# Kernel optimization log

Measured on AMD Instinct MI355X. Metric: run time of the kernel, lower is better.

## Reference

```python
import jax, jax.numpy as jnp
import numpy as np
from jax import lax

PCR = (-59.9, -59.9, -2.0, 59.9, 59.9, 5.9)
TOPK = 10
THRESHOLD = 0.5
MARGIN = 0.5
EPS = 1e-8  # torch cosine_similarity default eps


def setup_inputs() -> dict:
    key = jax.random.key(0)
    k1, k2, k3, k4, k5 = jax.random.split(key, 5)
    B, C, H, W, N = 4, 64, 512, 512, 30
    loc_features = jax.random.normal(k1, (B, C, H, W), dtype=jnp.float32)
    det_features = jax.random.normal(k2, (B, C, H, W), dtype=jnp.float32)
    # gt boxes: x,y inside point-cloud range; last element is class id (0 == static)
    xy = jax.random.uniform(k3, (B, N, 2), minval=-55.0, maxval=55.0, dtype=jnp.float32)
    rest = jax.random.normal(k4, (B, N, 5), dtype=jnp.float32)
    cls = jax.random.randint(k5, (B, N, 1), 0, 3).astype(jnp.float32)
    gt_boxes = jnp.concatenate([xy, rest, cls], axis=-1)  # [B, N, 8]
    return {"loc_features": loc_features, "det_features": det_features, "gt_boxes": gt_boxes}


def _loss_fwd(loc_features, det_features, gt_boxes):
    B, C, H, W = loc_features.shape
    bw = PCR[3] - PCR[0]
    bh = PCR[4] - PCR[1]

    def per_batch(loc_fm, det_fm, boxes):
        # --- static GT detection features (gather at box centers) ---
        static_mask = boxes[:, -1] == 0  # [N]
        cx = jnp.clip(((boxes[:, 0] - PCR[0]) / bw * W).astype(jnp.int32), 0, W - 1)
        cy = jnp.clip(((boxes[:, 1] - PCR[1]) / bh * H).astype(jnp.int32), 0, H - 1)
        det_feats = det_fm[:, cy, cx].T  # [N, C]

        # --- find_peaks: local-max of L2 intensity, threshold, top-k (stop-grad) ---
        intensity = lax.stop_gradient(jnp.sqrt(jnp.sum(loc_fm * loc_fm, axis=0)))  # [H, W]
        pooled = lax.reduce_window(intensity, -jnp.inf, lax.max, (3, 3), (1, 1), [(1, 1), (1, 1)])
        peak_mask = (intensity == pooled) & (intensity > THRESHOLD)
        masked = jnp.where(peak_mask, intensity, -jnp.inf).reshape(-1)
        vals, idx = lax.top_k(masked, TOPK)  # descending by intensity
        valid_peak = jnp.isfinite(vals)  # handles < TOPK peaks
        py, px = idx // W, idx % W
        peak_feats = loc_fm[:, py, px].T  # [K, C]

        # --- pairwise cosine similarity (torch eps semantics) ---
        dn = det_feats / jnp.maximum(jnp.linalg.norm(det_feats, axis=-1, keepdims=True), EPS)
        pn = peak_feats / jnp.maximum(jnp.linalg.norm(peak_feats, axis=-1, keepdims=True), EPS)
        sim = jnp.einsum('nc,kc->nk', dn, pn)  # [N, K]

        pair_mask = (static_mask[:, None] & valid_peak[None, :]).astype(sim.dtype)
        n_pairs = jnp.sum(pair_mask)
        loss_sum = jnp.sum(jax.nn.relu(sim - MARGIN) * pair_mask)
        return jnp.where(n_pairs > 0, loss_sum / jnp.maximum(n_pairs, 1.0), 0.0)

    losses = jax.vmap(per_batch)(loc_features, det_features, gt_boxes)  # [B]
    return jnp.sum(losses) / B


def reference(loc_features, det_features, gt_boxes):
    return _loss_fwd(loc_features, det_features, gt_boxes)
```

## Files before the change

kernel.cpp:

```cpp
#include <hip/hip_runtime.h>
#include <math.h>

typedef unsigned long long u64;
typedef unsigned int u32;
typedef float f4 __attribute__((ext_vector_type(4)));

#define HH 512
#define WW 512
#define CC 64
#define HWHW (HH * WW)
#define NBOX 30
#define KTOP 10
#define BLKS_PER_B 256
#define CAND_PER_BATCH (BLKS_PER_B * KTOP)

__device__ __forceinline__ u64 umax64(u64 a, u64 b) { return a > b ? a : b; }
__device__ __forceinline__ u64 umin64(u64 a, u64 b) { return a > b ? b : a; }

__device__ __forceinline__ void merge10(u64 lv[KTOP], const u64* B) {
    u64 c[16];
    #pragma unroll
    for (int i = 0; i < 16; ++i) {
        u64 a = (i < KTOP) ? lv[i] : 0ull;
        u64 b = (i >= 6) ? B[15 - i] : 0ull;
        c[i] = umax64(a, b);
    }
    #pragma unroll
    for (int s = 8; s >= 1; s >>= 1) {
        #pragma unroll
        for (int i = 0; i < 16; ++i) {
            if ((i & s) == 0) {
                u64 lo = c[i], hi = c[i | s];
                c[i] = umax64(lo, hi);
                c[i | s] = umin64(lo, hi);
            }
        }
    }
    #pragma unroll
    for (int i = 0; i < KTOP; ++i) lv[i] = c[i];
}

__global__ void k_intensity(const float* __restrict__ loc, float* __restrict__ inten) {
    int t   = threadIdx.x;
    int blk = blockIdx.x;
    int b   = blk >> 7;
    int j   = blk & 127;
    const f4* base = reinterpret_cast<const f4*>(loc + (size_t)b * CC * HWHW);
    int q0 = j * 512 + t;
    int q1 = q0 + 256;

    f4 s0 = {0.f, 0.f, 0.f, 0.f};
    f4 s1 = {0.f, 0.f, 0.f, 0.f};
    #pragma unroll 8
    for (int c = 0; c < CC; ++c) {
        const f4* p = base + (size_t)c * (HWHW / 4);
        f4 v0 = __builtin_nontemporal_load(p + q0);
        f4 v1 = __builtin_nontemporal_load(p + q1);
        s0 += v0 * v0;
        s1 += v1 * v1;
    }
    f4 o0, o1;
    o0[0] = sqrtf(s0[0]); o0[1] = sqrtf(s0[1]); o0[2] = sqrtf(s0[2]); o0[3] = sqrtf(s0[3]);
    o1[0] = sqrtf(s1[0]); o1[1] = sqrtf(s1[1]); o1[2] = sqrtf(s1[2]); o1[3] = sqrtf(s1[3]);
    f4* out = reinterpret_cast<f4*>(inten + (size_t)b * HWHW);
    out[q0] = o0;
    out[q1] = o1;
}

__global__ void k_peakblock(const float* __restrict__ inten, u64* __restrict__ cand) {
    int t    = threadIdx.x;
    int lane = t & 63;
    int blk  = blockIdx.x;
    int b    = blk >> 8;
    int pblk = blk & 255;
    const float* I = inten + (size_t)b * HWHW;
    int pix0 = pblk * 1024 + t * 4;
    int y  = pix0 >> 9;
    int x0 = pix0 & (WW - 1);

    float w00,w01,w02,w03,w04,w05, w10,w11,w12,w13,w14,w15, w20,w21,w22,w23,w24,w25;
    {
        bool r0 = (y - 1) >= 0, r2 = (y + 1) < HH;
        bool c0 = (x0 - 1) >= 0, c5 = (x0 + 4) < WW;
        const float* Rm = I + (y - 1) * WW + x0;
        const float* Rc = I + y * WW + x0;
        const float* Rp = I + (y + 1) * WW + x0;
        w00 = (r0 && c0) ? Rm[-1] : -INFINITY;
        w01 = r0 ? Rm[0] : -INFINITY;  w02 = r0 ? Rm[1] : -INFINITY;
        w03 = r0 ? Rm[2] : -INFINITY;  w04 = r0 ? Rm[3] : -INFINITY;
        w05 = (r0 && c5) ? Rm[4] : -INFINITY;
        w10 = c0 ? Rc[-1] : -INFINITY;
        w11 = Rc[0]; w12 = Rc[1]; w13 = Rc[2]; w14 = Rc[3];
        w15 = c5 ? Rc[4] : -INFINITY;
        w20 = (r2 && c0) ? Rp[-1] : -INFINITY;
        w21 = r2 ? Rp[0] : -INFINITY;  w22 = r2 ? Rp[1] : -INFINITY;
        w23 = r2 ? Rp[2] : -INFINITY;  w24 = r2 ? Rp[3] : -INFINITY;
        w25 = (r2 && c5) ? Rp[4] : -INFINITY;
    }

    u64 k0, k1, k2, k3;
    {
        float m, v;
        v = w11;
        m = fmaxf(fmaxf(fmaxf(w00, w01), fmaxf(w02, w10)),
                  fmaxf(fmaxf(w11, w12), fmaxf(fmaxf(w20, w21), w22)));
        k0 = (v > 0.5f && v == m) ? (((u64)(__float_as_uint(v) | 0x80000000u) << 32) | (u32)(~(u32)(pix0 + 0))) : 0ull;
        v = w12;
        m = fmaxf(fmaxf(fmaxf(w01, w02), fmaxf(w03, w11)),
                  fmaxf(fmaxf(w12, w13), fmaxf(fmaxf(w21, w22), w23)));
        k1 = (v > 0.5f && v == m) ? (((u64)(__float_as_uint(v) | 0x80000000u) << 32) | (u32)(~(u32)(pix0 + 1))) : 0ull;
        v = w13;
        m = fmaxf(fmaxf(fmaxf(w02, w03), fmaxf(w04, w12)),
                  fmaxf(fmaxf(w13, w14), fmaxf(fmaxf(w22, w23), w24)));
        k2 = (v > 0.5f && v == m) ? (((u64)(__float_as_uint(v) | 0x80000000u) << 32) | (u32)(~(u32)(pix0 + 2))) : 0ull;
        v = w14;
        m = fmaxf(fmaxf(fmaxf(w03, w04), fmaxf(w05, w13)),
                  fmaxf(fmaxf(w14, w15), fmaxf(fmaxf(w23, w24), w25)));
        k3 = (v > 0.5f && v == m) ? (((u64)(__float_as_uint(v) | 0x80000000u) << 32) | (u32)(~(u32)(pix0 + 3))) : 0ull;
    }

    u64 a[4]; int n = 0;
    if (k0) a[n++] = k0;
    if (k1) a[n++] = k1;
    if (k2) a[n++] = k2;
    if (k3) a[n++] = k3;

    __shared__ int cnt;
    __shared__ u64 pool[1024];
    __shared__ u64 smb[64][KTOP];
    if (t == 0) cnt = 0;
    __syncthreads();

    int incl = n;
    #pragma unroll
    for (int s = 1; s < 64; s <<= 1) {
        int o = __shfl_up(incl, s, 64);
        if (lane >= s) incl += o;
    }
    int excl = incl - n;
    int wtot = __shfl(incl, 63, 64);
    int base = 0;
    if (lane == 0 && wtot > 0) base = atomicAdd(&cnt, wtot);
    base = __shfl(base, 0, 64);
    for (int i = 0; i < n; ++i) pool[base + excl + i] = a[i];
    __syncthreads();

    int total = cnt;
    if (t < 64) {
        u64 lv[KTOP];
        #pragma unroll
        for (int i = 0; i < KTOP; ++i) lv[i] = 0ull;
        for (int j = lane; j < total; j += 64) {
            u64 v = pool[j];
            if (v > lv[KTOP - 1]) {
                lv[KTOP - 1] = v;
                #pragma unroll
                for (int m = KTOP - 1; m > 0; --m)
                    if (lv[m] > lv[m - 1]) { u64 tm = lv[m]; lv[m] = lv[m - 1]; lv[m - 1] = tm; }
            }
        }
        #pragma unroll
        for (int i = 0; i < KTOP; ++i) smb[lane][i] = lv[i];
        #pragma unroll
        for (int half = 32; half >= 1; half >>= 1) {
            if (lane < half) {
                merge10(lv, &smb[lane + half][0]);
                #pragma unroll
                for (int i = 0; i < KTOP; ++i) smb[lane][i] = lv[i];
            }
        }
        if (lane == 0) {
            u64* out = cand + (size_t)b * CAND_PER_BATCH + (size_t)pblk * KTOP;
            #pragma unroll
            for (int i = 0; i < KTOP; ++i) out[i] = lv[i];
        }
    }
}

__global__ void k_loss(const float* __restrict__ loc, const float* __restrict__ det,
                       const float* __restrict__ boxes,
                       const u64* __restrict__ cand,
                       float* __restrict__ bloss) {
    int b = blockIdx.x;
    int t = threadIdx.x;

    u64 lv[KTOP];
    #pragma unroll
    for (int i = 0; i < KTOP; ++i) lv[i] = 0ull;
    const u64* C = cand + (size_t)b * CAND_PER_BATCH;
    #pragma unroll
    for (int w = 0; w < CAND_PER_BATCH / 256; ++w) {
        u64 v = C[t + w * 256];
        if (v > lv[KTOP - 1]) {
            lv[KTOP - 1] = v;
            #pragma unroll
            for (int m = KTOP - 1; m > 0; --m)
                if (lv[m] > lv[m - 1]) { u64 tm = lv[m]; lv[m] = lv[m - 1]; lv[m - 1] = tm; }
        }
    }

    __shared__ u64 mb[256][KTOP];
    #pragma unroll
    for (int i = 0; i < KTOP; ++i) mb[t][i] = lv[i];
    __syncthreads();
    for (int half = 128; half >= 1; half >>= 1) {
        if (t < half) {
            merge10(lv, &mb[t + half][0]);
            #pragma unroll
            for (int i = 0; i < KTOP; ++i) mb[t][i] = lv[i];
        }
        __syncthreads();
    }

    __shared__ int topi[KTOP], tvalid[KTOP];
    if (t < KTOP) {
        u64 kk = mb[0][t];
        tvalid[t] = (kk != 0ull) ? 1 : 0;
        topi[t] = (int)((~(u32)kk) & (HWHW - 1));
    }

    __shared__ int s_cx[NBOX], s_cy[NBOX], s_static[NBOX];
    if (t < NBOX) {
        const float* bx = boxes + ((size_t)b * NBOX + t) * 8;
        float fx = (bx[0] + 59.9f) / 119.8f * 512.0f;
        float fy = (bx[1] + 59.9f) / 119.8f * 512.0f;
        int cx = (int)fx; int cy = (int)fy;
        cx = min(max(cx, 0), WW - 1);
        cy = min(max(cy, 0), HH - 1);
        s_cx[t] = cx; s_cy[t] = cy;
        s_static[t] = (bx[7] == 0.0f) ? 1 : 0;
    }
    __syncthreads();

    __shared__ float pf[KTOP][CC];
    __shared__ float df[NBOX][CC];
    #pragma unroll
    for (int w = 0; w < 3; ++w) {
        int e = t + w * 256;
        if (e < KTOP * CC) {
            int k = e >> 6, c = e & 63;
            int pix = tvalid[k] ? topi[k] : 0;
            pf[k][c] = loc[((size_t)b * CC + c) * HWHW + pix];
        }
    }
    #pragma unroll
    for (int w = 0; w < 8; ++w) {
        int e = t + w * 256;
        if (e < NBOX * CC) {
            int n = e >> 6, c = e & 63;
            int pix = s_cy[n] * WW + s_cx[n];
            df[n][c] = det[((size_t)b * CC + c) * HWHW + pix];
        }
    }
    __syncthreads();

    __shared__ float invn[NBOX + KTOP];
    if (t < NBOX + KTOP) {
        float s = 0.f;
        if (t < NBOX) {
            for (int c = 0; c < CC; ++c) s += df[t][c] * df[t][c];
        } else {
            int k = t - NBOX;
            for (int c = 0; c < CC; ++c) s += pf[k][c] * pf[k][c];
        }
        invn[t] = 1.0f / fmaxf(sqrtf(s), 1e-8f);
    }
    __syncthreads();
    for (int e = t; e < NBOX * CC; e += 256) { int n = e >> 6; df[n][e & 63] *= invn[n]; }
    for (int e = t; e < KTOP * CC; e += 256) { int k = e >> 6; pf[k][e & 63] *= invn[NBOX + k]; }
    __syncthreads();

    float lsum = 0.f, cntp = 0.f;
    for (int p = t; p < NBOX * KTOP; p += 256) {
        int n = p / KTOP, k = p - n * KTOP;
        float dot = 0.f;
        for (int c = 0; c < CC; ++c) dot += df[n][c] * pf[k][c];
        if (s_static[n] && tvalid[k]) {
            float r = dot - 0.5f;
            if (r > 0.f) lsum += r;
            cntp += 1.f;
        }
    }
    __shared__ float hv[256];
    __shared__ float hc[256];
    hv[t] = lsum; hc[t] = cntp;
    __syncthreads();
    for (int s = 128; s > 0; s >>= 1) {
        if (t < s) { hv[t] += hv[t + s]; hc[t] += hc[t + s]; }
        __syncthreads();
    }
    if (t == 0) {
        float np = hc[0];
        bloss[b] = (np > 0.f) ? hv[0] / fmaxf(np, 1.0f) : 0.f;
    }
}

__global__ void k_final(const float* __restrict__ bloss, float* __restrict__ out, int B) {
    float s = 0.f;
    for (int b = 0; b < B; ++b) s += bloss[b];
    out[0] = s / (float)B;
}

extern "C" void kernel_launch(void* const* d_in, const int* in_sizes, int n_in,
                              void* d_out, int out_size, void* d_ws, size_t ws_size,
                              hipStream_t stream) {
    const float* loc   = (const float*)d_in[0];
    const float* det   = (const float*)d_in[1];
    const float* boxes = (const float*)d_in[2];
    float* out = (float*)d_out;

    int B = in_sizes[0] / (CC * HWHW);

    float* inten = (float*)d_ws;
    u64*   cand  = (u64*)(inten + (size_t)B * HWHW);
    float* bloss = (float*)(cand + (size_t)B * CAND_PER_BATCH);

    dim3 blk(256);
    int g1 = B * 128;
    hipLaunchKernelGGL(k_intensity, dim3(g1), blk, 0, stream, loc, inten);
    hipLaunchKernelGGL(k_peakblock, dim3(B * BLKS_PER_B), blk, 0, stream, inten, cand);
    hipLaunchKernelGGL(k_loss, dim3(B), blk, 0, stream, loc, det, boxes, cand, bloss);
    hipLaunchKernelGGL(k_final, dim3(1), dim3(1), 0, stream, bloss, out, B);
}
```

Measured before the change: 75.77 us.

## Defer per-block top-k to loss kernel and fold final reduction via atomic

The peak kernel no longer reduces each block's candidates to a top-10. Each block writes its raw peak keys into a fixed per-block slot, spilling to an atomic overflow buffer when the slot is full. The loss kernel then has each thread scan one block's slot serially, and the separate final-sum kernel is replaced by a last-block-done atomic counter. This removes the shared-memory merge tree and one kernel launch, but adds serial scans of roughly a hundred strided loads per thread in a kernel that runs only B blocks, which may expose memory latency.

```diff
diff --git a/kernel.cpp b/kernel.cpp
--- a/kernel.cpp
+++ b/kernel.cpp
@@ -11,8 +11,8 @@
 #define HWHW (HH * WW)
 #define NBOX 30
 #define KTOP 10
-#define BLKS_PER_B 256
-#define CAND_PER_BATCH (BLKS_PER_B * KTOP)
+#define NBLK 256
+#define SLOT 256
 
 __device__ __forceinline__ u64 umax64(u64 a, u64 b) { return a > b ? a : b; }
 __device__ __forceinline__ u64 umin64(u64 a, u64 b) { return a > b ? b : a; }
@@ -40,7 +40,10 @@
     for (int i = 0; i < KTOP; ++i) lv[i] = c[i];
 }
 
-__global__ void k_intensity(const float* __restrict__ loc, float* __restrict__ inten) {
+__global__ void k_intensity(const float* __restrict__ loc, float* __restrict__ inten,
+                            int* __restrict__ ctrl, int B) {
+    if (blockIdx.x == 0 && threadIdx.x <= (unsigned)B) ctrl[threadIdx.x] = 0;
+
     int t   = threadIdx.x;
     int blk = blockIdx.x;
     int b   = blk >> 7;
@@ -67,9 +70,12 @@
     out[q1] = o1;
 }
 
-__global__ void k_peakblock(const float* __restrict__ inten, u64* __restrict__ cand) {
+__global__ void k_peakblock(const float* __restrict__ inten,
+                            u64* __restrict__ keys, int* __restrict__ counts,
+                            u64* __restrict__ ovf, int* __restrict__ ctrl) {
     int t    = threadIdx.x;
     int lane = t & 63;
+    int wid  = t >> 6;
     int blk  = blockIdx.x;
     int b    = blk >> 8;
     int pblk = blk & 255;
@@ -125,12 +131,7 @@
     if (k2) a[n++] = k2;
     if (k3) a[n++] = k3;
 
-    __shared__ int cnt;
-    __shared__ u64 pool[1024];
-    __shared__ u64 smb[64][KTOP];
-    if (t == 0) cnt = 0;
-    __syncthreads();
-
+    __shared__ int wsum[4];
     int incl = n;
     #pragma unroll
     for (int s = 1; s < 64; s <<= 1) {
@@ -138,20 +139,47 @@
         if (lane >= s) incl += o;
     }
     int excl = incl - n;
-    int wtot = __shfl(incl, 63, 64);
-    int base = 0;
-    if (lane == 0 && wtot > 0) base = atomicAdd(&cnt, wtot);
-    base = __shfl(base, 0, 64);
-    for (int i = 0; i < n; ++i) pool[base + excl + i] = a[i];
-    __syncthreads();
-
-    int total = cnt;
-    if (t < 64) {
-        u64 lv[KTOP];
-        #pragma unroll
-        for (int i = 0; i < KTOP; ++i) lv[i] = 0ull;
-        for (int j = lane; j < total; j += 64) {
-            u64 v = pool[j];
+    if (lane == 63) wsum[wid] = incl;
+    __syncthreads();
+    int woff = 0, total = 0;
+    #pragma unroll
+    for (int w = 0; w < 4; ++w) {
+        int v = wsum[w];
+        if (w < wid) woff += v;
+        total += v;
+    }
+    int base = woff + excl;
+
+    u64* slot = keys + ((size_t)b * NBLK + pblk) * SLOT;
+    for (int i = 0; i < n; ++i) {
+        int p = base + i;
+        if (p < SLOT) {
+            slot[p] = a[i];
+        } else {
+            int op = atomicAdd(&ctrl[b], 1);
+            ovf[(size_t)b * HWHW + op] = a[i];
+        }
+    }
+    if (t == 0) counts[b * NBLK + pblk] = total;
+}
+
+__global__ void k_loss(const float* __restrict__ loc, const float* __restrict__ det,
+                       const float* __restrict__ boxes,
+                       const u64* __restrict__ keys, const int* __restrict__ counts,
+                       const u64* __restrict__ ovf, int* __restrict__ ctrl,
+                       float* __restrict__ bloss, float* __restrict__ out, int B) {
+    int b = blockIdx.x;
+    int t = threadIdx.x;
+
+    u64 lv[KTOP];
+    #pragma unroll
+    for (int i = 0; i < KTOP; ++i) lv[i] = 0ull;
+    {
+        const u64* slot = keys + ((size_t)b * NBLK + t) * SLOT;
+        int cn = counts[b * NBLK + t];
+        int lim = cn < SLOT ? cn : SLOT;
+        for (int i = 0; i < lim; ++i) {
+            u64 v = slot[i];
             if (v > lv[KTOP - 1]) {
                 lv[KTOP - 1] = v;
                 #pragma unroll
@@ -159,43 +187,15 @@
                     if (lv[m] > lv[m - 1]) { u64 tm = lv[m]; lv[m] = lv[m - 1]; lv[m - 1] = tm; }
             }
         }
-        #pragma unroll
-        for (int i = 0; i < KTOP; ++i) smb[lane][i] = lv[i];
-        #pragma unroll
-        for (int half = 32; half >= 1; half >>= 1) {
-            if (lane < half) {
-                merge10(lv, &smb[lane + half][0]);
+        int oc = ctrl[b];
+        for (int j = t; j < oc; j += 256) {
+            u64 v = ovf[(size_t)b * HWHW + j];
+            if (v > lv[KTOP - 1]) {
+                lv[KTOP - 1] = v;
                 #pragma unroll
-                for (int i = 0; i < KTOP; ++i) smb[lane][i] = lv[i];
+                for (int m = KTOP - 1; m > 0; --m)
+                    if (lv[m] > lv[m - 1]) { u64 tm = lv[m]; lv[m] = lv[m - 1]; lv[m - 1] = tm; }
             }
-        }
-        if (lane == 0) {
-            u64* out = cand + (size_t)b * CAND_PER_BATCH + (size_t)pblk * KTOP;
-            #pragma unroll
-            for (int i = 0; i < KTOP; ++i) out[i] = lv[i];
-        }
-    }
-}
-
-__global__ void k_loss(const float* __restrict__ loc, const float* __restrict__ det,
-                       const float* __restrict__ boxes,
-                       const u64* __restrict__ cand,
-                       float* __restrict__ bloss) {
-    int b = blockIdx.x;
-    int t = threadIdx.x;
-
-    u64 lv[KTOP];
-    #pragma unroll
-    for (int i = 0; i < KTOP; ++i) lv[i] = 0ull;
-    const u64* C = cand + (size_t)b * CAND_PER_BATCH;
-    #pragma unroll
-    for (int w = 0; w < CAND_PER_BATCH / 256; ++w) {
-        u64 v = C[t + w * 256];
-        if (v > lv[KTOP - 1]) {
-            lv[KTOP - 1] = v;
-            #pragma unroll
-            for (int m = KTOP - 1; m > 0; --m)
-                if (lv[m] > lv[m - 1]) { u64 tm = lv[m]; lv[m] = lv[m - 1]; lv[m - 1] = tm; }
         }
     }
 
@@ -292,13 +292,15 @@
     if (t == 0) {
         float np = hc[0];
         bloss[b] = (np > 0.f) ? hv[0] / fmaxf(np, 1.0f) : 0.f;
-    }
-}
-
-__global__ void k_final(const float* __restrict__ bloss, float* __restrict__ out, int B) {
-    float s = 0.f;
-    for (int b = 0; b < B; ++b) s += bloss[b];
-    out[0] = s / (float)B;
+        __threadfence();
+        int old = atomicAdd(&ctrl[B], 1);
+        if (old == B - 1) {
+            __threadfence();
+            float s = 0.f;
+            for (int i = 0; i < B; ++i) s += bloss[i];
+            out[0] = s / (float)B;
+        }
+    }
 }
 
 extern "C" void kernel_launch(void* const* d_in, const int* in_sizes, int n_in,
@@ -312,13 +314,14 @@
     int B = in_sizes[0] / (CC * HWHW);
 
     float* inten = (float*)d_ws;
-    u64*   cand  = (u64*)(inten + (size_t)B * HWHW);
-    float* bloss = (float*)(cand + (size_t)B * CAND_PER_BATCH);
+    u64*   keys  = (u64*)(inten + (size_t)B * HWHW);
+    u64*   ovf   = keys + (size_t)B * NBLK * SLOT;
+    int*   counts= (int*)(ovf + (size_t)B * HWHW);
+    int*   ctrl  = counts + B * NBLK;
+    float* bloss = (float*)(ctrl + B + 1);
 
     dim3 blk(256);
-    int g1 = B * 128;
-    hipLaunchKernelGGL(k_intensity, dim3(g1), blk, 0, stream, loc, inten);
-    hipLaunchKernelGGL(k_peakblock, dim3(B * BLKS_PER_B), blk, 0, stream, inten, cand);
-    hipLaunchKernelGGL(k_loss, dim3(B), blk, 0, stream, loc, det, boxes, cand, bloss);
-    hipLaunchKernelGGL(k_final, dim3(1), dim3(1), 0, stream, bloss, out, B);
-}
+    hipLaunchKernelGGL(k_intensity, dim3(B * 128), blk, 0, stream, loc, inten, ctrl, B);
+    hipLaunchKernelGGL(k_peakblock, dim3(B * NBLK), blk, 0, stream, inten, keys, counts, ovf, ctrl);
+    hipLaunchKernelGGL(k_loss, dim3(B), blk, 0, stream, loc, det, boxes, keys, counts, ovf, ctrl, bloss, out, B);
+}
```

Result: slower. 114.4 us (+51.0%).
